# Kernel optimization log

Hardware: AMD Instinct MI355X
Metric: run time of the kernel (lower is better)

Reference implementation:

```python
import jax, jax.numpy as jnp
import numpy as np

B, L, D = 16, 1024, 512   # batch, input_seq_len, d_model
H, DH = 8, 64             # ac_heads, d_model // ac_heads (= d_v)
C_FACTOR = 2              # config['c']


def setup_inputs() -> dict:
    key = jax.random.key(0)
    ks = jax.random.split(key, 5)
    Q = jax.random.normal(ks[0], (B, L, D), jnp.float32)
    K = jax.random.normal(ks[1], (B, L, D), jnp.float32)
    V = jax.random.normal(ks[2], (B, L, D), jnp.float32)
    Wq = jax.random.normal(ks[3], (D, DH), jnp.float32) * (1.0 / np.sqrt(D))
    bq = jax.random.normal(ks[4], (DH,), jnp.float32) * 0.02
    return {"Q": Q, "K": K, "V": V, "Wq": Wq, "bq": bq}


def reference(Q, K, V, Wq, bq):
    B_, L_, D_ = Q.shape
    dh = Wq.shape[1]
    heads = D_ // dh
    # The source reuses self.query for Q, K and V projections (keys/values
    # Dense layers are dead code), so one shared (Wq, bq) is faithful.
    q = Q @ Wq + bq   # [B, L, dh]
    k_ = K @ Wq + bq
    v = V @ Wq + bq
    # Source stacks `heads` identical copies of the same projection, then
    # transposes to [B, H, dh, L]; broadcast instead of recomputing.
    to_heads = lambda x: jnp.broadcast_to(
        jnp.swapaxes(x, 1, 2)[:, None], (B_, heads, dh, L_))
    qh = to_heads(q).astype(jnp.complex64)
    kh = to_heads(k_).astype(jnp.complex64)
    vh = to_heads(v)
    # FFT-based circular cross-correlation along the time axis
    corr = jnp.real(jnp.fft.ifft(jnp.fft.fft(qh) * jnp.conj(jnp.fft.fft(kh))))  # [B,H,dh,L]
    ktop = int(C_FACTOR * np.log(L_))
    vals, idxs = jax.lax.top_k(corr, ktop)          # [B,H,dh,k]
    w = jax.nn.softmax(vals, axis=-1)               # softmax over the k lags
    # tf.roll(v, shift=-idx)[j] == v[(j + idx) mod L]: one gather per lag
    pos = (idxs[..., None] + jnp.arange(L_)) % L_    # [B,H,dh,k,L]
    vg = jnp.take_along_axis(vh[..., None, :], pos, axis=-1)  # [B,H,dh,k,L]
    agg = jnp.sum(w[..., None] * vg, axis=-2)        # [B,H,dh,L]
    # reshape to [B, d_model, L] then transpose -> [B, L, d_model]
    return jnp.swapaxes(agg.reshape(B_, heads * dh, L_), 1, 2)
```

## Files before the change

### kernel.cpp

```cpp
#include <hip/hip_runtime.h>
#include <float.h>
#include <math.h>

#define PROJ_N (16*64*1024)

using short8_t  = __attribute__((ext_vector_type(8)))  short;
using uint4_t   = __attribute__((ext_vector_type(4)))  unsigned;
using floatx16  = __attribute__((ext_vector_type(16))) float;

__global__ __launch_bounds__(256) void proj_kernel(
    const float* __restrict__ Q, const float* __restrict__ K,
    const float* __restrict__ V, const float* __restrict__ Wq,
    const float* __restrict__ bq, float* __restrict__ proj) {
  __shared__ float XsT[64 * 64];
  __shared__ float Ws[64 * 64];

  const int blk  = blockIdx.x;
  const int in   = blk >> 8;
  const int row0 = (blk & 255) << 6;
  const float* __restrict__ X = (in == 0) ? Q : (in == 1 ? K : V);

  const int t  = threadIdx.x;
  const int c4 = t & 15;
  const int rr = t >> 4;
  const int tx = t & 15;
  const int ty = t >> 4;

  float acc[4][4] = {{0.f,0.f,0.f,0.f},{0.f,0.f,0.f,0.f},
                     {0.f,0.f,0.f,0.f},{0.f,0.f,0.f,0.f}};

  for (int kt = 0; kt < 8; ++kt) {
    const int k0 = kt << 6;
    __syncthreads();
#pragma unroll
    for (int it = 0; it < 4; ++it) {
      const int r = it * 16 + rr;
      float4 f = *(const float4*)&X[(size_t)(row0 + r) * 512 + k0 + 4 * c4];
      const int sw = ((((r >> 2) ^ (c4 & 7)) << 2) | (r & 3));
      XsT[(4 * c4 + 0) * 64 + sw] = f.x;
      XsT[(4 * c4 + 1) * 64 + sw] = f.y;
      XsT[(4 * c4 + 2) * 64 + sw] = f.z;
      XsT[(4 * c4 + 3) * 64 + sw] = f.w;
      float4 g = *(const float4*)&Wq[(size_t)(k0 + r) * 64 + 4 * c4];
      *(float4*)&Ws[r * 64 + 4 * c4] = g;
    }
    __syncthreads();

#pragma unroll 4
    for (int kk = 0; kk < 64; ++kk) {
      const int sk = (kk >> 2) & 7;
      float4 x4 = *(float4*)&XsT[kk * 64 + ((ty ^ sk) << 2)];
      float4 wv = *(float4*)&Ws[kk * 64 + 4 * tx];
      acc[0][0] += x4.x * wv.x; acc[0][1] += x4.x * wv.y;
      acc[0][2] += x4.x * wv.z; acc[0][3] += x4.x * wv.w;
      acc[1][0] += x4.y * wv.x; acc[1][1] += x4.y * wv.y;
      acc[1][2] += x4.y * wv.z; acc[1][3] += x4.y * wv.w;
      acc[2][0] += x4.z * wv.x; acc[2][1] += x4.z * wv.y;
      acc[2][2] += x4.z * wv.z; acc[2][3] += x4.z * wv.w;
      acc[3][0] += x4.w * wv.x; acc[3][1] += x4.w * wv.y;
      acc[3][2] += x4.w * wv.z; acc[3][3] += x4.w * wv.w;
    }
  }

  const int b  = row0 >> 10;
  const int l0 = row0 & 1023;
  float* __restrict__ op = proj + (size_t)in * PROJ_N + (size_t)(b * 64) * 1024;
#pragma unroll
  for (int j = 0; j < 4; ++j) {
    const int d = 4 * tx + j;
    const float bias = bq[d];
    float4 o = make_float4(acc[0][j] + bias, acc[1][j] + bias,
                           acc[2][j] + bias, acc[3][j] + bias);
    *(float4*)&op[(size_t)d * 1024 + l0 + 4 * ty] = o;
  }
}

__device__ __forceinline__ unsigned bf16r(float x) {
  unsigned u = __float_as_uint(x);
  return (u + 0x7FFFu + ((u >> 16) & 1u)) >> 16;
}
__device__ __forceinline__ unsigned pk_bf16(float x, float y) {
  return bf16r(x) | (bf16r(y) << 16);
}

__global__ __launch_bounds__(256) void corr_mfma_kernel(
    const float* __restrict__ qp, const float* __restrict__ kp,
    float* __restrict__ wvals, int* __restrict__ widx) {
  __shared__ __align__(16) short qh[2048];
  __shared__ __align__(16) short ql[2048];
  __shared__ __align__(16) short kh[2048];
  __shared__ __align__(16) short kl[2048];
  __shared__ float corr4[4][1024];
  __shared__ float tv[13];
  __shared__ int   ts[13];
  __shared__ float rv[4];
  __shared__ int   rs[4];
  __shared__ int   bsh;

  const int pair = blockIdx.x;
  const int tid  = threadIdx.x;
  const int w    = tid >> 6;
  const int lane = tid & 63;
  const int row  = lane & 31;
  const int hk   = lane >> 5;

  const float* __restrict__ qg = qp + (size_t)pair * 1024;
  const float* __restrict__ kg = kp + (size_t)pair * 1024;

  {
    const int j = (tid << 3) & 1023;
    float4 a0 = *(const float4*)&qg[j];
    float4 a1 = *(const float4*)&qg[j + 4];
    float fq[8] = {a0.x, a0.y, a0.z, a0.w, a1.x, a1.y, a1.z, a1.w};
    unsigned hb[8]; float lf[8];
#pragma unroll
    for (int m = 0; m < 8; ++m) {
      hb[m] = bf16r(fq[m]);
      lf[m] = fq[m] - __uint_as_float(hb[m] << 16);
    }
    uint4_t vqh = { hb[0] | (hb[1] << 16), hb[2] | (hb[3] << 16),
                    hb[4] | (hb[5] << 16), hb[6] | (hb[7] << 16) };
    uint4_t vql = { pk_bf16(lf[0], lf[1]), pk_bf16(lf[2], lf[3]),
                    pk_bf16(lf[4], lf[5]), pk_bf16(lf[6], lf[7]) };
    *(uint4_t*)&qh[tid << 3] = vqh;
    *(uint4_t*)&ql[tid << 3] = vql;

    float4 b0 = *(const float4*)&kg[j];
    float4 b1 = *(const float4*)&kg[j + 4];
    float fk[8] = {b0.x, b0.y, b0.z, b0.w, b1.x, b1.y, b1.z, b1.w};
#pragma unroll
    for (int m = 0; m < 8; ++m) {
      hb[m] = bf16r(fk[m]);
      lf[m] = fk[m] - __uint_as_float(hb[m] << 16);
    }
    uint4_t vkh = { hb[0] | (hb[1] << 16), hb[2] | (hb[3] << 16),
                    hb[4] | (hb[5] << 16), hb[6] | (hb[7] << 16) };
    uint4_t vkl = { pk_bf16(lf[0], lf[1]), pk_bf16(lf[2], lf[3]),
                    pk_bf16(lf[4], lf[5]), pk_bf16(lf[6], lf[7]) };
    const int p = tid ^ ((tid >> 3) & 7);
    *(uint4_t*)&kh[p << 3] = vkh;
    *(uint4_t*)&kl[p << 3] = vkl;
  }
  __syncthreads();

  floatx16 acc = {0.f,0.f,0.f,0.f,0.f,0.f,0.f,0.f,
                  0.f,0.f,0.f,0.f,0.f,0.f,0.f,0.f};
  const unsigned* __restrict__ qhd = (const unsigned*)qh;
  const unsigned* __restrict__ qld = (const unsigned*)ql;
#pragma unroll
  for (int i = 0; i < 16; ++i) {
    const int k0 = (w << 8) + (i << 4);
    const int e0 = 1024 + k0 + (hk << 3) - (row << 5);
    const int c  = e0 >> 3;
    const int p  = c ^ ((c >> 3) & 7);
    short8_t ah = *(const short8_t*)&kh[p << 3];
    short8_t al = *(const short8_t*)&kl[p << 3];
    const int s0 = k0 + (hk << 3) + row;
    const int d0 = s0 >> 1;
    const unsigned sh = (s0 & 1) << 4;
    unsigned w0 = qhd[d0 + 0], w1 = qhd[d0 + 1], w2 = qhd[d0 + 2],
             w3 = qhd[d0 + 3], w4 = qhd[d0 + 4];
    uint4_t buh = { __builtin_amdgcn_alignbit(w1, w0, sh),
                    __builtin_amdgcn_alignbit(w2, w1, sh),
                    __builtin_amdgcn_alignbit(w3, w2, sh),
                    __builtin_amdgcn_alignbit(w4, w3, sh) };
    unsigned x0 = qld[d0 + 0], x1 = qld[d0 + 1], x2 = qld[d0 + 2],
             x3 = qld[d0 + 3], x4 = qld[d0 + 4];
    uint4_t bul = { __builtin_amdgcn_alignbit(x1, x0, sh),
                    __builtin_amdgcn_alignbit(x2, x1, sh),
                    __builtin_amdgcn_alignbit(x3, x2, sh),
                    __builtin_amdgcn_alignbit(x4, x3, sh) };
    short8_t bh = __builtin_bit_cast(short8_t, buh);
    short8_t bl = __builtin_bit_cast(short8_t, bul);
    acc = __builtin_amdgcn_mfma_f32_32x32x16_bf16(ah, bh, acc, 0, 0, 0);
    acc = __builtin_amdgcn_mfma_f32_32x32x16_bf16(ah, bl, acc, 0, 0, 0);
    acc = __builtin_amdgcn_mfma_f32_32x32x16_bf16(al, bh, acc, 0, 0, 0);
  }

#pragma unroll
  for (int r = 0; r < 16; ++r) {
    const int srow = (r & 3) + ((r >> 2) << 3) + (hk << 2);
    corr4[w][(srow << 5) | row] = acc[r];
  }
  __syncthreads();

  float v0 = corr4[0][tid]       + corr4[1][tid]       + corr4[2][tid]       + corr4[3][tid];
  float v1 = corr4[0][tid + 256] + corr4[1][tid + 256] + corr4[2][tid + 256] + corr4[3][tid + 256];
  float v2 = corr4[0][tid + 512] + corr4[1][tid + 512] + corr4[2][tid + 512] + corr4[3][tid + 512];
  float v3 = corr4[0][tid + 768] + corr4[1][tid + 768] + corr4[2][tid + 768] + corr4[3][tid + 768];

  for (int r = 0; r < 13; ++r) {
    float bv = v0; int bs = tid;
    if (v1 > bv) { bv = v1; bs = tid + 256; }
    if (v2 > bv) { bv = v2; bs = tid + 512; }
    if (v3 > bv) { bv = v3; bs = tid + 768; }
#pragma unroll
    for (int off = 32; off >= 1; off >>= 1) {
      float ov = __shfl_xor(bv, off, 64);
      int   os = __shfl_xor(bs, off, 64);
      if (ov > bv || (ov == bv && os < bs)) { bv = ov; bs = os; }
    }
    if (lane == 0) { rv[w] = bv; rs[w] = bs; }
    __syncthreads();
    if (tid == 0) {
      float cv = rv[0]; int cs = rs[0];
#pragma unroll
      for (int u = 1; u < 4; ++u)
        if (rv[u] > cv || (rv[u] == cv && rs[u] < cs)) { cv = rv[u]; cs = rs[u]; }
      tv[r] = cv; ts[r] = cs; bsh = cs;
    }
    __syncthreads();
    const int bw = bsh;
    if ((bw & 255) == tid) {
      const int slot = bw >> 8;
      if      (slot == 0) v0 = -FLT_MAX;
      else if (slot == 1) v1 = -FLT_MAX;
      else if (slot == 2) v2 = -FLT_MAX;
      else                v3 = -FLT_MAX;
    }
  }

  if (tid == 0) {
    const float mx = tv[0];
    float e[13]; float s = 0.f;
#pragma unroll
    for (int k = 0; k < 13; ++k) { e[k] = __expf(tv[k] - mx); s += e[k]; }
    const float inv = 1.f / s;
#pragma unroll
    for (int k = 0; k < 13; ++k) {
      wvals[pair * 16 + k] = e[k] * inv;
      widx [pair * 16 + k] = ts[k];
    }
  }
}

__global__ __launch_bounds__(256) void agg_kernel(
    const float* __restrict__ vp, const float* __restrict__ wvals,
    const int* __restrict__ widx, float* __restrict__ agg) {
  __shared__ float vs[2048];
  __shared__ float wv[13];
  __shared__ int   wi[13];
  const int pair = blockIdx.x;
  const int t = threadIdx.x;
  const float* __restrict__ vg = vp + (size_t)pair * 1024;
  *(float4*)&vs[4 * t]         = *(const float4*)&vg[(4 * t) & 1023];
  *(float4*)&vs[4 * (t + 256)] = *(const float4*)&vg[(4 * (t + 256)) & 1023];
  if (t < 13) { wv[t] = wvals[pair * 16 + t]; wi[t] = widx[pair * 16 + t]; }
  __syncthreads();

  float r0 = 0.f, r1 = 0.f, r2 = 0.f, r3 = 0.f;
#pragma unroll
  for (int k = 0; k < 13; ++k) {
    const float wk = wv[k];
    const int   ik = wi[k];
    r0 += wk * vs[t        + ik];
    r1 += wk * vs[t + 256  + ik];
    r2 += wk * vs[t + 512  + ik];
    r3 += wk * vs[t + 768  + ik];
  }
  float* __restrict__ ag = agg + (size_t)pair * 1024;
  ag[t] = r0; ag[t + 256] = r1; ag[t + 512] = r2; ag[t + 768] = r3;
}

__global__ __launch_bounds__(256) void out_kernel(
    const float* __restrict__ agg, float* __restrict__ out) {
  __shared__ float tile[64][65];
  const int blk = blockIdx.x;
  const int b = blk >> 4, lt = blk & 15;
  const int l0 = lt * 64;
  const int t = threadIdx.x;
  const int j = t & 63, qq = t >> 6;

#pragma unroll
  for (int p = 0; p < 16; ++p) {
    const int d = p * 4 + qq;
    tile[d][j] = agg[(size_t)(b * 64 + d) * 1024 + l0 + j];
  }
  __syncthreads();
#pragma unroll
  for (int p = 0; p < 16; ++p) {
    const int jj = p * 4 + qq;
    const float val = tile[j][jj];
    const size_t rowbase = ((size_t)(b * 1024 + l0 + jj)) * 512;
#pragma unroll
    for (int h = 0; h < 8; ++h)
      out[rowbase + h * 64 + j] = val;
  }
}

extern "C" void kernel_launch(void* const* d_in, const int* in_sizes, int n_in,
                              void* d_out, int out_size, void* d_ws, size_t ws_size,
                              hipStream_t stream) {
  const float* Q  = (const float*)d_in[0];
  const float* K  = (const float*)d_in[1];
  const float* V  = (const float*)d_in[2];
  const float* Wq = (const float*)d_in[3];
  const float* bq = (const float*)d_in[4];
  float* out = (float*)d_out;
  float* ws  = (float*)d_ws;

  float* proj  = ws;
  float* agg   = ws + (size_t)3 * PROJ_N;
  float* wvals = ws + (size_t)4 * PROJ_N;
  int*   widx  = (int*)(ws + (size_t)4 * PROJ_N + 16384);

  proj_kernel<<<768, 256, 0, stream>>>(Q, K, V, Wq, bq, proj);
  corr_mfma_kernel<<<1024, 256, 0, stream>>>(proj, proj + PROJ_N, wvals, widx);
  agg_kernel<<<1024, 256, 0, stream>>>(proj + (size_t)2 * PROJ_N, wvals, widx, agg);
  out_kernel<<<256, 256, 0, stream>>>(agg, out);
}
```

Baseline: 188.7 us.

## Move projection to split-bf16 MFMA and fuse aggregation into correlation kernel

The projection GEMM changes from scalar FP32 FMA tiling to 32x32x16 bf16 MFMA. It keeps near-FP32 accuracy with a hi/lo split (three MFMAs per step), and a new small kernel pre-transposes and splits Wq into bf16 halves. The aggregation kernel is folded into the correlation kernel: V is staged into the reused corr4 shared buffer and the softmax weights and indices stay in shared memory. This removes one launch and the weights/indices round trip. The projection now reads X directly from global memory with no LDS staging and stores scattered per-element columns, so memory efficiency may drop.

```diff
diff --git a/kernel.cpp b/kernel.cpp
--- a/kernel.cpp
+++ b/kernel.cpp
@@ -8,90 +8,110 @@
 using uint4_t   = __attribute__((ext_vector_type(4)))  unsigned;
 using floatx16  = __attribute__((ext_vector_type(16))) float;
 
-__global__ __launch_bounds__(256) void proj_kernel(
+__device__ __forceinline__ unsigned bf16r(float x) {
+  unsigned u = __float_as_uint(x);
+  return (u + 0x7FFFu + ((u >> 16) & 1u)) >> 16;
+}
+__device__ __forceinline__ unsigned pk_bf16(float x, float y) {
+  return bf16r(x) | (bf16r(y) << 16);
+}
+__device__ __forceinline__ void split8(float4 a, float4 b, short8_t& h, short8_t& l) {
+  float f[8] = {a.x, a.y, a.z, a.w, b.x, b.y, b.z, b.w};
+  unsigned hp[4], lp[4];
+#pragma unroll
+  for (int j = 0; j < 4; ++j) {
+    unsigned h0 = bf16r(f[2*j]), h1 = bf16r(f[2*j+1]);
+    hp[j] = h0 | (h1 << 16);
+    float l0 = f[2*j]   - __uint_as_float(h0 << 16);
+    float l1 = f[2*j+1] - __uint_as_float(h1 << 16);
+    lp[j] = pk_bf16(l0, l1);
+  }
+  uint4_t hv = {hp[0], hp[1], hp[2], hp[3]};
+  uint4_t lv = {lp[0], lp[1], lp[2], lp[3]};
+  h = __builtin_bit_cast(short8_t, hv);
+  l = __builtin_bit_cast(short8_t, lv);
+}
+
+__global__ __launch_bounds__(256) void wtrans_kernel(
+    const float* __restrict__ Wq, unsigned short* __restrict__ Wth,
+    unsigned short* __restrict__ Wtl) {
+  const int tg = blockIdx.x * 256 + threadIdx.x;
+  const int d = tg & 63, k = tg >> 6;
+  const float x = Wq[k * 64 + d];
+  const unsigned h = bf16r(x);
+  const float lo = x - __uint_as_float(h << 16);
+  Wth[d * 512 + k] = (unsigned short)h;
+  Wtl[d * 512 + k] = (unsigned short)bf16r(lo);
+}
+
+__global__ __launch_bounds__(128) void proj_kernel(
     const float* __restrict__ Q, const float* __restrict__ K,
-    const float* __restrict__ V, const float* __restrict__ Wq,
-    const float* __restrict__ bq, float* __restrict__ proj) {
-  __shared__ float XsT[64 * 64];
-  __shared__ float Ws[64 * 64];
-
+    const float* __restrict__ V, const unsigned short* __restrict__ Wth,
+    const unsigned short* __restrict__ Wtl, const float* __restrict__ bq,
+    float* __restrict__ proj) {
   const int blk  = blockIdx.x;
   const int in   = blk >> 8;
   const int row0 = (blk & 255) << 6;
   const float* __restrict__ X = (in == 0) ? Q : (in == 1 ? K : V);
 
-  const int t  = threadIdx.x;
-  const int c4 = t & 15;
-  const int rr = t >> 4;
-  const int tx = t & 15;
-  const int ty = t >> 4;
-
-  float acc[4][4] = {{0.f,0.f,0.f,0.f},{0.f,0.f,0.f,0.f},
-                     {0.f,0.f,0.f,0.f},{0.f,0.f,0.f,0.f}};
-
-  for (int kt = 0; kt < 8; ++kt) {
-    const int k0 = kt << 6;
-    __syncthreads();
-#pragma unroll
-    for (int it = 0; it < 4; ++it) {
-      const int r = it * 16 + rr;
-      float4 f = *(const float4*)&X[(size_t)(row0 + r) * 512 + k0 + 4 * c4];
-      const int sw = ((((r >> 2) ^ (c4 & 7)) << 2) | (r & 3));
-      XsT[(4 * c4 + 0) * 64 + sw] = f.x;
-      XsT[(4 * c4 + 1) * 64 + sw] = f.y;
-      XsT[(4 * c4 + 2) * 64 + sw] = f.z;
-      XsT[(4 * c4 + 3) * 64 + sw] = f.w;
-      float4 g = *(const float4*)&Wq[(size_t)(k0 + r) * 64 + 4 * c4];
-      *(float4*)&Ws[r * 64 + 4 * c4] = g;
-    }
-    __syncthreads();
-
-#pragma unroll 4
-    for (int kk = 0; kk < 64; ++kk) {
-      const int sk = (kk >> 2) & 7;
-      float4 x4 = *(float4*)&XsT[kk * 64 + ((ty ^ sk) << 2)];
-      float4 wv = *(float4*)&Ws[kk * 64 + 4 * tx];
-      acc[0][0] += x4.x * wv.x; acc[0][1] += x4.x * wv.y;
-      acc[0][2] += x4.x * wv.z; acc[0][3] += x4.x * wv.w;
-      acc[1][0] += x4.y * wv.x; acc[1][1] += x4.y * wv.y;
-      acc[1][2] += x4.y * wv.z; acc[1][3] += x4.y * wv.w;
-      acc[2][0] += x4.z * wv.x; acc[2][1] += x4.z * wv.y;
-      acc[2][2] += x4.z * wv.z; acc[2][3] += x4.z * wv.w;
-      acc[3][0] += x4.w * wv.x; acc[3][1] += x4.w * wv.y;
-      acc[3][2] += x4.w * wv.z; acc[3][3] += x4.w * wv.w;
-    }
-  }
-
-  const int b  = row0 >> 10;
-  const int l0 = row0 & 1023;
-  float* __restrict__ op = proj + (size_t)in * PROJ_N + (size_t)(b * 64) * 1024;
-#pragma unroll
-  for (int j = 0; j < 4; ++j) {
-    const int d = 4 * tx + j;
-    const float bias = bq[d];
-    float4 o = make_float4(acc[0][j] + bias, acc[1][j] + bias,
-                           acc[2][j] + bias, acc[3][j] + bias);
-    *(float4*)&op[(size_t)d * 1024 + l0 + 4 * ty] = o;
-  }
-}
-
-__device__ __forceinline__ unsigned bf16r(float x) {
-  unsigned u = __float_as_uint(x);
-  return (u + 0x7FFFu + ((u >> 16) & 1u)) >> 16;
-}
-__device__ __forceinline__ unsigned pk_bf16(float x, float y) {
-  return bf16r(x) | (bf16r(y) << 16);
+  const int tid  = threadIdx.x;
+  const int w    = tid >> 6;
+  const int lane = tid & 63;
+  const int col  = lane & 31;
+  const int hk   = lane >> 5;
+
+  const int lrow = row0 + w * 32 + col;
+  const float* __restrict__ xrow = X + (size_t)lrow * 512;
+  const unsigned short* __restrict__ wh0 = Wth + (size_t)col * 512;
+  const unsigned short* __restrict__ wl0 = Wtl + (size_t)col * 512;
+  const unsigned short* __restrict__ wh1 = wh0 + 32 * 512;
+  const unsigned short* __restrict__ wl1 = wl0 + 32 * 512;
+
+  floatx16 acc0 = {0.f,0.f,0.f,0.f,0.f,0.f,0.f,0.f,
+                   0.f,0.f,0.f,0.f,0.f,0.f,0.f,0.f};
+  floatx16 acc1 = {0.f,0.f,0.f,0.f,0.f,0.f,0.f,0.f,
+                   0.f,0.f,0.f,0.f,0.f,0.f,0.f,0.f};
+
+#pragma unroll 2
+  for (int ks = 0; ks < 32; ++ks) {
+    const int k0 = ks * 16 + hk * 8;
+    float4 xa = *(const float4*)&xrow[k0];
+    float4 xb = *(const float4*)&xrow[k0 + 4];
+    short8_t a0h = *(const short8_t*)&wh0[k0];
+    short8_t a0l = *(const short8_t*)&wl0[k0];
+    short8_t a1h = *(const short8_t*)&wh1[k0];
+    short8_t a1l = *(const short8_t*)&wl1[k0];
+    short8_t bh, bl;
+    split8(xa, xb, bh, bl);
+    acc0 = __builtin_amdgcn_mfma_f32_32x32x16_bf16(a0h, bh, acc0, 0, 0, 0);
+    acc1 = __builtin_amdgcn_mfma_f32_32x32x16_bf16(a1h, bh, acc1, 0, 0, 0);
+    acc0 = __builtin_amdgcn_mfma_f32_32x32x16_bf16(a0h, bl, acc0, 0, 0, 0);
+    acc1 = __builtin_amdgcn_mfma_f32_32x32x16_bf16(a1h, bl, acc1, 0, 0, 0);
+    acc0 = __builtin_amdgcn_mfma_f32_32x32x16_bf16(a0l, bh, acc0, 0, 0, 0);
+    acc1 = __builtin_amdgcn_mfma_f32_32x32x16_bf16(a1l, bh, acc1, 0, 0, 0);
+  }
+
+  const int b    = lrow >> 10;
+  const int lloc = lrow & 1023;
+  float* __restrict__ p = proj + (size_t)in * PROJ_N + ((size_t)(b * 64) << 10) + lloc;
+#pragma unroll
+  for (int r = 0; r < 16; ++r) {
+    const int m = (r & 3) + ((r >> 2) << 3) + (hk << 2);
+    p[(size_t)m << 10]        = acc0[r] + bq[m];
+    p[(size_t)(m + 32) << 10] = acc1[r] + bq[m + 32];
+  }
 }
 
 __global__ __launch_bounds__(256) void corr_mfma_kernel(
     const float* __restrict__ qp, const float* __restrict__ kp,
-    float* __restrict__ wvals, int* __restrict__ widx) {
+    const float* __restrict__ vp, float* __restrict__ agg) {
   __shared__ __align__(16) short qh[2048];
   __shared__ __align__(16) short ql[2048];
   __shared__ __align__(16) short kh[2048];
   __shared__ __align__(16) short kl[2048];
   __shared__ float corr4[4][1024];
   __shared__ float tv[13];
+  __shared__ float sw[13];
   __shared__ int   ts[13];
   __shared__ float rv[4];
   __shared__ int   rs[4];
@@ -106,40 +126,22 @@
 
   const float* __restrict__ qg = qp + (size_t)pair * 1024;
   const float* __restrict__ kg = kp + (size_t)pair * 1024;
+  const float* __restrict__ vg = vp + (size_t)pair * 1024;
 
   {
     const int j = (tid << 3) & 1023;
     float4 a0 = *(const float4*)&qg[j];
     float4 a1 = *(const float4*)&qg[j + 4];
-    float fq[8] = {a0.x, a0.y, a0.z, a0.w, a1.x, a1.y, a1.z, a1.w};
-    unsigned hb[8]; float lf[8];
-#pragma unroll
-    for (int m = 0; m < 8; ++m) {
-      hb[m] = bf16r(fq[m]);
-      lf[m] = fq[m] - __uint_as_float(hb[m] << 16);
-    }
-    uint4_t vqh = { hb[0] | (hb[1] << 16), hb[2] | (hb[3] << 16),
-                    hb[4] | (hb[5] << 16), hb[6] | (hb[7] << 16) };
-    uint4_t vql = { pk_bf16(lf[0], lf[1]), pk_bf16(lf[2], lf[3]),
-                    pk_bf16(lf[4], lf[5]), pk_bf16(lf[6], lf[7]) };
-    *(uint4_t*)&qh[tid << 3] = vqh;
-    *(uint4_t*)&ql[tid << 3] = vql;
-
+    short8_t h8, l8;
+    split8(a0, a1, h8, l8);
+    *(short8_t*)&qh[tid << 3] = h8;
+    *(short8_t*)&ql[tid << 3] = l8;
     float4 b0 = *(const float4*)&kg[j];
     float4 b1 = *(const float4*)&kg[j + 4];
-    float fk[8] = {b0.x, b0.y, b0.z, b0.w, b1.x, b1.y, b1.z, b1.w};
-#pragma unroll
-    for (int m = 0; m < 8; ++m) {
-      hb[m] = bf16r(fk[m]);
-      lf[m] = fk[m] - __uint_as_float(hb[m] << 16);
-    }
-    uint4_t vkh = { hb[0] | (hb[1] << 16), hb[2] | (hb[3] << 16),
-                    hb[4] | (hb[5] << 16), hb[6] | (hb[7] << 16) };
-    uint4_t vkl = { pk_bf16(lf[0], lf[1]), pk_bf16(lf[2], lf[3]),
-                    pk_bf16(lf[4], lf[5]), pk_bf16(lf[6], lf[7]) };
+    split8(b0, b1, h8, l8);
     const int p = tid ^ ((tid >> 3) & 7);
-    *(uint4_t*)&kh[p << 3] = vkh;
-    *(uint4_t*)&kl[p << 3] = vkl;
+    *(short8_t*)&kh[p << 3] = h8;
+    *(short8_t*)&kl[p << 3] = l8;
   }
   __syncthreads();
 
@@ -184,10 +186,18 @@
   }
   __syncthreads();
 
+  float4 vl0 = *(const float4*)&vg[(4 * tid) & 1023];
+  float4 vl1 = *(const float4*)&vg[(4 * (tid + 256)) & 1023];
+
   float v0 = corr4[0][tid]       + corr4[1][tid]       + corr4[2][tid]       + corr4[3][tid];
   float v1 = corr4[0][tid + 256] + corr4[1][tid + 256] + corr4[2][tid + 256] + corr4[3][tid + 256];
   float v2 = corr4[0][tid + 512] + corr4[1][tid + 512] + corr4[2][tid + 512] + corr4[3][tid + 512];
   float v3 = corr4[0][tid + 768] + corr4[1][tid + 768] + corr4[2][tid + 768] + corr4[3][tid + 768];
+  __syncthreads();
+
+  float* vs = &corr4[0][0];
+  *(float4*)&vs[4 * tid]         = vl0;
+  *(float4*)&vs[4 * (tid + 256)] = vl1;
 
   for (int r = 0; r < 13; ++r) {
     float bv = v0; int bs = tid;
@@ -227,39 +237,22 @@
     for (int k = 0; k < 13; ++k) { e[k] = __expf(tv[k] - mx); s += e[k]; }
     const float inv = 1.f / s;
 #pragma unroll
-    for (int k = 0; k < 13; ++k) {
-      wvals[pair * 16 + k] = e[k] * inv;
-      widx [pair * 16 + k] = ts[k];
-    }
-  }
-}
-
-__global__ __launch_bounds__(256) void agg_kernel(
-    const float* __restrict__ vp, const float* __restrict__ wvals,
-    const int* __restrict__ widx, float* __restrict__ agg) {
-  __shared__ float vs[2048];
-  __shared__ float wv[13];
-  __shared__ int   wi[13];
-  const int pair = blockIdx.x;
-  const int t = threadIdx.x;
-  const float* __restrict__ vg = vp + (size_t)pair * 1024;
-  *(float4*)&vs[4 * t]         = *(const float4*)&vg[(4 * t) & 1023];
-  *(float4*)&vs[4 * (t + 256)] = *(const float4*)&vg[(4 * (t + 256)) & 1023];
-  if (t < 13) { wv[t] = wvals[pair * 16 + t]; wi[t] = widx[pair * 16 + t]; }
+    for (int k = 0; k < 13; ++k) sw[k] = e[k] * inv;
+  }
   __syncthreads();
 
   float r0 = 0.f, r1 = 0.f, r2 = 0.f, r3 = 0.f;
 #pragma unroll
-  for (int k = 0; k < 13; ++k) {
-    const float wk = wv[k];
-    const int   ik = wi[k];
-    r0 += wk * vs[t        + ik];
-    r1 += wk * vs[t + 256  + ik];
-    r2 += wk * vs[t + 512  + ik];
-    r3 += wk * vs[t + 768  + ik];
+  for (int k2 = 0; k2 < 13; ++k2) {
+    const float wk = sw[k2];
+    const int   ik = ts[k2];
+    r0 += wk * vs[tid        + ik];
+    r1 += wk * vs[tid + 256  + ik];
+    r2 += wk * vs[tid + 512  + ik];
+    r3 += wk * vs[tid + 768  + ik];
   }
   float* __restrict__ ag = agg + (size_t)pair * 1024;
-  ag[t] = r0; ag[t + 256] = r1; ag[t + 512] = r2; ag[t + 768] = r3;
+  ag[tid] = r0; ag[tid + 256] = r1; ag[tid + 512] = r2; ag[tid + 768] = r3;
 }
 
 __global__ __launch_bounds__(256) void out_kernel(
@@ -299,13 +292,14 @@
   float* out = (float*)d_out;
   float* ws  = (float*)d_ws;
 
-  float* proj  = ws;
-  float* agg   = ws + (size_t)3 * PROJ_N;
-  float* wvals = ws + (size_t)4 * PROJ_N;
-  int*   widx  = (int*)(ws + (size_t)4 * PROJ_N + 16384);
-
-  proj_kernel<<<768, 256, 0, stream>>>(Q, K, V, Wq, bq, proj);
-  corr_mfma_kernel<<<1024, 256, 0, stream>>>(proj, proj + PROJ_N, wvals, widx);
-  agg_kernel<<<1024, 256, 0, stream>>>(proj + (size_t)2 * PROJ_N, wvals, widx, agg);
+  float* proj = ws;
+  float* agg  = ws + (size_t)3 * PROJ_N;
+  unsigned short* Wth = (unsigned short*)agg;
+  unsigned short* Wtl = Wth + 64 * 512;
+
+  wtrans_kernel<<<128, 256, 0, stream>>>(Wq, Wth, Wtl);
+  proj_kernel<<<768, 128, 0, stream>>>(Q, K, V, Wth, Wtl, bq, proj);
+  corr_mfma_kernel<<<1024, 256, 0, stream>>>(proj, proj + PROJ_N,
+                                             proj + (size_t)2 * PROJ_N, agg);
   out_kernel<<<256, 256, 0, stream>>>(agg, out);
 }
```

After: 186.9 us. Within noise of the previous version (-1.0%).
